# Kernel optimization log

Measured on AMD Instinct MI355X. Metric: run time of the kernel, lower is better.

## Reference

```python
import jax, jax.numpy as jnp
import numpy as np

# graph sizes
G, P, EP = 128, 256, 1024          # graphs, nodes/graph, edges/graph
N, E = G * P, G * EP
C, KENS, S = 4, 2, 1               # centroids, ensembles, samples
R = S * KENS                       # repeats
F, DE, D, OUT = 64, 16, 128, 10


def setup_inputs() -> dict:
    key = jax.random.key(0)
    ks = jax.random.split(key, 24)
    off = (jnp.arange(G, dtype=jnp.int32) * P)[:, None]
    src = (jax.random.randint(ks[0], (G, EP), 0, P, dtype=jnp.int32) + off).reshape(-1)
    dst = (jax.random.randint(ks[1], (G, EP), 0, P, dtype=jnp.int32) + off).reshape(-1)
    edge_index = jnp.stack([src, dst])            # [2, E], edges stay within graphs
    batch = jnp.repeat(jnp.arange(G, dtype=jnp.int32), P)  # [N]
    rn = lambda k, shp, s: jax.random.normal(k, shp, jnp.float32) * s
    return {
        "x_feat": rn(ks[2], (N, F), 1.0),
        "edge_attr": rn(ks[3], (E, DE), 1.0),
        "W_atom": rn(ks[4], (F, D), 0.1), "b_atom": jnp.zeros((D,), jnp.float32),
        "W_score": rn(ks[5], (D, C * KENS), 0.1),
        "W_edge": rn(ks[6], (DE, D), 0.1),
        "W_b2c": rn(ks[7], (D, D), 0.1),
        "W_bb": rn(ks[8], (D, D), 0.1), "W_bc": rn(ks[9], (D, D), 0.1),
        "W_cb": rn(ks[10], (D, D), 0.1), "W_cc": rn(ks[11], (D, D), 0.1),
        "W_sb": rn(ks[12], (D, D), 0.1), "W_sc": rn(ks[13], (D, D), 0.1),
        "W_inter": rn(ks[14], (D, D), 0.1), "b_inter": jnp.zeros((D,), jnp.float32),
        "W_out": rn(ks[15], (D, OUT), 0.1), "b_out": jnp.zeros((OUT,), jnp.float32),
        "edge_index": edge_index, "batch": batch,
    }


def reference(x_feat, edge_attr, W_atom, b_atom, W_score, W_edge, W_b2c,
              W_bb, W_bc, W_cb, W_cc, W_sb, W_sc, W_inter, b_inter,
              W_out, b_out, edge_index, batch):
    src, dst = edge_index[0], edge_index[1]
    # atom encoder + scorer + softmax sampler (marginals)
    x = x_feat @ W_atom + b_atom                                  # [N,D]
    scores = (x @ W_score).reshape(N, C, KENS)
    marg = jax.nn.softmax(scores, axis=1)                         # over centroids
    nm = jnp.broadcast_to(marg[None], (S, N, C, KENS))            # [S,N,C,KENS]
    nm = jnp.transpose(nm, (0, 3, 2, 1)).reshape(R, C, N)         # [R,C,N]
    em = nm[:, :, src] * nm[:, :, dst]                            # edge_mask [R,C,E]
    # base2centroid: masked MP on base graph + weighted segment-mean pooling
    edge_emb = edge_attr @ W_edge                                 # [E,D]
    h = jax.nn.relu(x @ W_b2c)                                    # [N,D]
    m = h[src] + edge_emb                                         # [E,D]
    agg = jnp.zeros((R, C, N, D), m.dtype).at[:, :, dst].add(em[..., None] * m)
    hm = h[None, None] + agg                                      # [R,C,N,D]
    denom = jnp.zeros((R, C, G), nm.dtype).at[:, :, batch].add(nm)
    num = jnp.zeros((R, C, G, D), hm.dtype).at[:, :, batch].add(nm[..., None] * hm)
    cent_x = jnp.transpose(num / (denom[..., None] + 1e-6), (0, 2, 1, 3))  # [R,G,C,D]
    # intra centroid-pair edge weights: triu pairs + diag, scatter over graphs
    iu, ju = np.triu_indices(C, 1)
    pi = np.concatenate([iu, np.arange(C)])
    pj = np.concatenate([ju, np.arange(C)])
    e2g = batch[src]
    w = jnp.zeros((R, pi.size, G), nm.dtype).at[:, :, e2g].add(
        nm[:, pi][:, :, src] * nm[:, pj][:, :, dst])              # [R,10,G]
    w = w.at[:, -C:, :].multiply(0.5)                             # halve diagonal counts
    wt = jnp.transpose(w, (0, 2, 1))                              # [R,G,10]
    Wcc = jnp.zeros((R, G, C, C), nm.dtype)
    Wcc = Wcc.at[:, :, pi, pj].add(wt).at[:, :, pj, pi].add(wt)   # to_undirected
    dg = jnp.arange(C)
    Wcc = Wcc.at[:, :, dg, dg].multiply(0.5)                      # self loops counted once
    Wcc = Wcc / (jax.lax.stop_gradient(jnp.max(Wcc)) + 1e-9)      # detached-max norm
    # hetero GNN layer: base->base, base->centroid, centroid->centroid, centroid->base
    agg_bb = jnp.zeros((N, D), x.dtype).at[dst].add(x[src] + edge_emb)           # [N,D]
    agg_bc = jnp.transpose(
        jnp.zeros((R, C, G, D), x.dtype).at[:, :, batch].add(nm[..., None] * x[None, None]),
        (0, 2, 1, 3))                                             # [R,G,C,D]
    agg_cc = jnp.einsum('rgij,rgjd->rgid', Wcc, cent_x)
    h_cent = jax.nn.relu(agg_bc @ W_bc + agg_cc @ W_cc + cent_x @ W_sc)          # [R,G,C,D]
    agg_cb = jnp.einsum('rcn,rncd->rnd', nm, h_cent[:, batch])                   # [R,N,D]
    h_base = jax.nn.relu(agg_bb[None] @ W_bb + agg_cb @ W_cb + x[None] @ W_sb)   # [R,N,D]
    # inter-ensemble mean pool, inter head, intra mean graph pool, intra head
    node_emb = jnp.mean(h_base, axis=0) @ W_inter + b_inter                      # [N,D]
    graph_emb = jnp.zeros((G, D), node_emb.dtype).at[batch].add(node_emb) / P    # [G,D]
    return graph_emb @ W_out + b_out                                             # [G,OUT]
```

## Files before the change

### kernel.cpp

```cpp
#include <hip/hip_runtime.h>
#include <hip/hip_bf16.h>

#define Nn 32768
#define Ee 131072
#define Gg 128
#define Dd 128

using bf16 = __hip_bfloat16;
typedef __attribute__((ext_vector_type(8))) short bf16x8;
typedef __attribute__((ext_vector_type(4))) float f32x4;

__device__ __forceinline__ float b2f(bf16 v){ return __bfloat162float(v); }
__device__ __forceinline__ bf16  f2b(float v){ return __float2bfloat16(v); }
__device__ __forceinline__ unsigned short bf16bits(float v){
  union { bf16 b; unsigned short u; } cv; cv.b = f2b(v); return cv.u;
}
__device__ __forceinline__ float bfu(unsigned short u){
  return __uint_as_float((unsigned int)u << 16);
}
__device__ __forceinline__ float upk_x(unsigned int v){ return __uint_as_float(v << 16); }
__device__ __forceinline__ float upk_h(unsigned int v){ return __uint_as_float(v & 0xffff0000u); }

__global__ __launch_bounds__(128)
void k_wrep(const float* __restrict__ Wbb, const float* __restrict__ Wsb,
            const float* __restrict__ Wcb, const float* __restrict__ Wa,
            const float* __restrict__ Wb2c,
            unsigned short* __restrict__ Wbbp, unsigned short* __restrict__ Wsbp,
            unsigned short* __restrict__ Wcbp, unsigned short* __restrict__ Wap,
            unsigned short* __restrict__ Wb2cp) {
  int mat = blockIdx.x >> 7, n = blockIdx.x & 127, k = threadIdx.x;
  if      (mat == 0) Wbbp [n*128 + k] = bf16bits(Wbb [k*128 + n]);
  else if (mat == 1) Wsbp [n*128 + k] = bf16bits(Wsb [k*128 + n]);
  else if (mat == 2) Wcbp [n*128 + k] = bf16bits(Wcb [k*128 + n]);
  else if (mat == 3) { if (k < 64) Wap[n*64 + k] = bf16bits(Wa[k*128 + n]); }
  else               Wb2cp[n*128 + k] = bf16bits(Wb2c[k*128 + n]);
}

__global__ __launch_bounds__(256)
void k_atom(const float* __restrict__ xf, const unsigned short* __restrict__ Wap,
            const float* __restrict__ ba, const float* __restrict__ Wsc,
            const unsigned short* __restrict__ Wb2cp,
            unsigned int* __restrict__ xh, float* __restrict__ nmt) {
  __shared__ unsigned short sxf[64*72];
  __shared__ unsigned short sxb[64*136];
  __shared__ float ss[64*8];
  __shared__ float sWsc[1024];
  int tid = threadIdx.x, n0 = blockIdx.x*64;
  int lane = tid & 63, wv = tid >> 6;
  int m = lane & 15, quad = lane >> 4;
  int rbase = wv*16;
  #pragma unroll
  for (int k = 0; k < 4; ++k) {
    int pos = (tid + k*256)*4;
    int node = pos >> 6, f = pos & 63;
    float4 v = *reinterpret_cast<const float4*>(xf + (size_t)n0*64 + pos);
    ushort4 o;
    o.x = bf16bits(v.x); o.y = bf16bits(v.y); o.z = bf16bits(v.z); o.w = bf16bits(v.w);
    *reinterpret_cast<ushort4*>(&sxf[node*72 + f]) = o;
  }
  for (int j = tid; j < 1024; j += 256) sWsc[j] = Wsc[j];
  __syncthreads();
  f32x4 cx[8];
  #pragma unroll
  for (int nt = 0; nt < 8; ++nt) {
    float bv = ba[nt*16 + m];
    cx[nt] = (f32x4){bv, bv, bv, bv};
  }
  const unsigned short* a1 = &sxf[(rbase + m)*72];
  #pragma unroll
  for (int nt = 0; nt < 8; ++nt) {
    #pragma unroll
    for (int kk = 0; kk < 2; ++kk) {
      int ko = kk*32 + quad*8;
      bf16x8 av = *reinterpret_cast<const bf16x8*>((const short*)a1 + ko);
      bf16x8 bv8 = *reinterpret_cast<const bf16x8*>((const short*)Wap + (nt*16 + m)*64 + ko);
      cx[nt] = __builtin_amdgcn_mfma_f32_16x16x32_bf16(av, bv8, cx[nt], 0, 0, 0);
    }
  }
  #pragma unroll
  for (int nt = 0; nt < 8; ++nt)
    #pragma unroll
    for (int i = 0; i < 4; ++i)
      sxb[(rbase + quad*4 + i)*136 + nt*16 + m] = bf16bits(cx[nt][i]);
  __syncthreads();
  for (int p = tid; p < 512; p += 256) {
    int node = p >> 3, col = p & 7;
    float s = 0.f;
    for (int dd = 0; dd < 128; ++dd)
      s += bfu(sxb[node*136 + dd]) * sWsc[dd*8 + col];
    ss[node*8 + col] = s;
  }
  __syncthreads();
  if (tid < 128) {
    int node = tid >> 1, k = tid & 1;
    float v0 = ss[node*8 + 0 + k], v1 = ss[node*8 + 2 + k];
    float v2 = ss[node*8 + 4 + k], v3 = ss[node*8 + 6 + k];
    float mx = fmaxf(fmaxf(v0, v1), fmaxf(v2, v3));
    float e0 = expf(v0-mx), e1 = expf(v1-mx), e2 = expf(v2-mx), e3 = expf(v3-mx);
    float inv = 1.f / (e0+e1+e2+e3);
    *reinterpret_cast<float4*>(nmt + (size_t)(n0 + node)*8 + k*4) =
        make_float4(e0*inv, e1*inv, e2*inv, e3*inv);
  }
  f32x4 chf[8];
  #pragma unroll
  for (int nt = 0; nt < 8; ++nt) chf[nt] = (f32x4){0.f,0.f,0.f,0.f};
  const unsigned short* a2 = &sxb[(rbase + m)*136];
  #pragma unroll
  for (int nt = 0; nt < 8; ++nt) {
    #pragma unroll
    for (int kk = 0; kk < 4; ++kk) {
      int ko = kk*32 + quad*8;
      bf16x8 av = *reinterpret_cast<const bf16x8*>((const short*)a2 + ko);
      bf16x8 bv8 = *reinterpret_cast<const bf16x8*>((const short*)Wb2cp + (nt*16 + m)*128 + ko);
      chf[nt] = __builtin_amdgcn_mfma_f32_16x16x32_bf16(av, bv8, chf[nt], 0, 0, 0);
    }
  }
  #pragma unroll
  for (int nt = 0; nt < 8; ++nt) {
    #pragma unroll
    for (int i = 0; i < 4; ++i) {
      int row = rbase + quad*4 + i, col = nt*16 + m;
      float hv = fmaxf(chf[nt][i], 0.f);
      unsigned short xb = sxb[row*136 + col];
      xh[(size_t)(n0 + row)*128 + col] =
          ((unsigned int)bf16bits(hv) << 16) | (unsigned int)xb;
    }
  }
}

__global__ __launch_bounds__(256)
void k_graph(const int* __restrict__ ei, const float* __restrict__ nmt,
             const float* __restrict__ ea,
             int* __restrict__ osrc, int* __restrict__ rowstart,
             float* __restrict__ sea, float* __restrict__ den,
             float* __restrict__ wcc, unsigned int* __restrict__ maxbits,
             float* __restrict__ bnm, float* __restrict__ gea) {
  __shared__ int sdl[1024], ssl[1024];
  __shared__ int cnt[256], off[256];
  __shared__ float eabuf[256*16];
  __shared__ float salpha[8*258];
  __shared__ float sbeta[8*256];
  __shared__ float seaacc[256*17];
  __shared__ float red[20];
  __shared__ float sga[256];
  __shared__ float den8[8];
  int t = threadIdx.x, g = blockIdx.x;
  cnt[t] = 0;
  for (int j = t; j < 2048; j += 256) sbeta[j] = 0.f;
  for (int j = t; j < 4352; j += 256) seaacc[j] = 0.f;
  if (t < 20) red[t] = 0.f;
  if (t < 8) den8[t] = 0.f;
  __syncthreads();
  #pragma unroll
  for (int j = 0; j < 4; ++j) {
    int e = t + j*256;
    int sl = ei[g*1024 + e] - g*256;
    int dl = ei[Ee + g*1024 + e] - g*256;
    ssl[e] = sl; sdl[e] = dl;
    atomicAdd(&cnt[dl], 1);
  }
  {
    const float4* p = reinterpret_cast<const float4*>(nmt + (size_t)(g*256 + t)*8);
    float4 a = p[0], b = p[1];
    float v[8] = {a.x,a.y,a.z,a.w,b.x,b.y,b.z,b.w};
    #pragma unroll
    for (int i = 0; i < 8; ++i) {
      float s = v[i];
      for (int o = 32; o > 0; o >>= 1) s += __shfl_xor(s, o);
      if ((t & 63) == 0) atomicAdd(&den8[i], s);
    }
  }
  __syncthreads();
  off[t] = cnt[t];
  __syncthreads();
  for (int s = 1; s < 256; s <<= 1) {
    int v = (t >= s) ? off[t - s] : 0;
    __syncthreads();
    off[t] += v;
    __syncthreads();
  }
  int startv = off[t] - cnt[t];
  rowstart[g*256 + t] = startv;
  off[t] = startv;
  __syncthreads();
  #pragma unroll
  for (int j = 0; j < 4; ++j) {
    int e = t + j*256;
    int pos = atomicAdd(&off[sdl[e]], 1);
    osrc[g*1024 + pos] = g*256 + ssl[e];
  }
  float w20[20];
  #pragma unroll
  for (int i = 0; i < 20; ++i) w20[i] = 0.f;
  float greg = 0.f;
  int grc = t >> 5, gj = (t >> 1) & 15, ghf = t & 1;
  for (int ch = 0; ch < 4; ++ch) {
    __syncthreads();
    for (int j = t; j < 1024; j += 256)
      reinterpret_cast<float4*>(eabuf)[j] =
        reinterpret_cast<const float4*>(ea + (size_t)(g*1024 + ch*256)*16)[j];
    {
      int e = ch*256 + t;
      int sl = ssl[e], dl = sdl[e];
      const float4* ps4 = reinterpret_cast<const float4*>(nmt + (size_t)(g*256 + sl)*8);
      const float4* pt4 = reinterpret_cast<const float4*>(nmt + (size_t)(g*256 + dl)*8);
      float4 sv0 = ps4[0], sv1 = ps4[1], tv0 = pt4[0], tv1 = pt4[1];
      float ps[8] = {sv0.x,sv0.y,sv0.z,sv0.w,sv1.x,sv1.y,sv1.z,sv1.w};
      float pt[8] = {tv0.x,tv0.y,tv0.z,tv0.w,tv1.x,tv1.y,tv1.z,tv1.w};
      #pragma unroll
      for (int r = 0; r < 2; ++r) {
        int b = r*4;
        w20[r*10+0] += ps[b+0]*pt[b+1]; w20[r*10+1] += ps[b+0]*pt[b+2];
        w20[r*10+2] += ps[b+0]*pt[b+3]; w20[r*10+3] += ps[b+1]*pt[b+2];
        w20[r*10+4] += ps[b+1]*pt[b+3]; w20[r*10+5] += ps[b+2]*pt[b+3];
        w20[r*10+6] += ps[b+0]*pt[b+0]; w20[r*10+7] += ps[b+1]*pt[b+1];
        w20[r*10+8] += ps[b+2]*pt[b+2]; w20[r*10+9] += ps[b+3]*pt[b+3];
      }
      #pragma unroll
      for (int rc = 0; rc < 8; ++rc) {
        float al = ps[rc]*pt[rc]*pt[rc];
        salpha[rc*258 + t] = al;
        atomicAdd(&sbeta[rc*256 + sl], al);
      }
    }
    __syncthreads();
    {
      int e = ch*256 + t;
      int dl = sdl[e];
      #pragma unroll
      for (int j2 = 0; j2 < 16; ++j2)
        atomicAdd(&seaacc[dl*17 + j2], eabuf[t*16 + j2]);
    }
    {
      float a = 0.f;
      int eb = ghf*128;
      for (int ee = eb; ee < eb + 128; ++ee)
        a += salpha[grc*258 + ee] * eabuf[ee*16 + gj];
      greg += a;
    }
  }
  #pragma unroll
  for (int i = 0; i < 20; ++i) {
    for (int o = 32; o > 0; o >>= 1) w20[i] += __shfl_down(w20[i], o);
  }
  if ((t & 63) == 0) {
    #pragma unroll
    for (int i = 0; i < 20; ++i) atomicAdd(&red[i], w20[i]);
  }
  sga[t] = greg;
  __syncthreads();
  if (t < 32) {
    int r = t >> 4, ij = t & 15, i = ij >> 2, j = ij & 3;
    float v;
    if (i == j) v = 0.5f * red[r*10 + 6 + i];
    else { int a = i < j ? i : j, b = i < j ? j : i;
           int p = (a == 0) ? (b - 1) : (a == 1) ? (b + 1) : 5;
           v = red[r*10 + p]; }
    wcc[(r*Gg + g)*16 + ij] = v;
    atomicMax(maxbits, __float_as_uint(v));
  }
  if ((t & 1) == 0) {
    float s = sga[t] + sga[t+1];
    gea[((size_t)grc*Gg + g)*16 + gj] = s;
  }
  {
    float4* bo = reinterpret_cast<float4*>(bnm + (size_t)(g*256 + t)*8);
    bo[0] = make_float4(sbeta[0*256+t], sbeta[1*256+t], sbeta[2*256+t], sbeta[3*256+t]);
    bo[1] = make_float4(sbeta[4*256+t], sbeta[5*256+t], sbeta[6*256+t], sbeta[7*256+t]);
  }
  {
    float4* so = reinterpret_cast<float4*>(sea + (size_t)(g*256 + t)*16);
    so[0] = make_float4(seaacc[t*17+0],  seaacc[t*17+1],  seaacc[t*17+2],  seaacc[t*17+3]);
    so[1] = make_float4(seaacc[t*17+4],  seaacc[t*17+5],  seaacc[t*17+6],  seaacc[t*17+7]);
    so[2] = make_float4(seaacc[t*17+8],  seaacc[t*17+9],  seaacc[t*17+10], seaacc[t*17+11]);
    so[3] = make_float4(seaacc[t*17+12], seaacc[t*17+13], seaacc[t*17+14], seaacc[t*17+15]);
  }
  if (t < 8) den[t*Gg + g] = den8[t];
}

__global__ __launch_bounds__(256)
void k_pool(const unsigned int* __restrict__ xh, const float* __restrict__ nmt,
            const float* __restrict__ bnm, float* __restrict__ pnum,
            float* __restrict__ pabc) {
  __shared__ float combN[8*128], combA[8*128];
  int t = threadIdx.x, d = t & 127, q = t >> 7;
  int g = blockIdx.x >> 4, e16 = blockIdx.x & 15;
  int nbase = g*256 + e16*16;
  float aH[8] = {0,0,0,0,0,0,0,0};
  float aX[8] = {0,0,0,0,0,0,0,0};
  for (int nn = q; nn < 16; nn += 2) {
    int n = nbase + nn;
    unsigned int vn = xh[(size_t)n*128 + d];
    float xn = upk_x(vn), hn = upk_h(vn);
    const float4* pp = reinterpret_cast<const float4*>(nmt + (size_t)n*8);
    float4 p0 = pp[0], p1 = pp[1];
    float pc[8] = {p0.x,p0.y,p0.z,p0.w,p1.x,p1.y,p1.z,p1.w};
    const float4* bp = reinterpret_cast<const float4*>(bnm + (size_t)n*8);
    float4 b0 = bp[0], b1 = bp[1];
    float bt[8] = {b0.x,b0.y,b0.z,b0.w,b1.x,b1.y,b1.z,b1.w};
    #pragma unroll
    for (int rc = 0; rc < 8; ++rc) {
      aH[rc] += (pc[rc] + bt[rc])*hn;
      aX[rc] += pc[rc]*xn;
    }
  }
  if (q == 1) {
    #pragma unroll
    for (int rc = 0; rc < 8; ++rc) { combN[rc*128+d] = aH[rc]; combA[rc*128+d] = aX[rc]; }
  }
  __syncthreads();
  if (q == 0) {
    #pragma unroll
    for (int rc = 0; rc < 8; ++rc) {
      pnum[(((size_t)rc*Gg + g)*16 + e16)*128 + d] = aH[rc] + combN[rc*128+d];
      pabc[(((size_t)rc*Gg + g)*16 + e16)*128 + d] = aX[rc] + combA[rc*128+d];
    }
  }
}

__global__ __launch_bounds__(256)
void k_aggx(const unsigned int* __restrict__ xh, const float* __restrict__ sea,
            const float* __restrict__ We, const int* __restrict__ osrc,
            const int* __restrict__ rowstart, unsigned short* __restrict__ aggbb16) {
  int t = threadIdx.x, d = t & 127, q = t >> 7;
  int g = blockIdx.x >> 5, e32 = blockIdx.x & 31;
  int nbase = g*256 + e32*8;
  float w[16];
  #pragma unroll
  for (int j = 0; j < 16; ++j) w[j] = We[j*128 + d];
  for (int nn = q; nn < 8; nn += 2) {
    int n = nbase + nn;
    const float4* sp = reinterpret_cast<const float4*>(sea + (size_t)n*16);
    float4 s0 = sp[0], s1 = sp[1], s2 = sp[2], s3 = sp[3];
    float agg = s0.x*w[0] + s0.y*w[1] + s0.z*w[2] + s0.w*w[3]
              + s1.x*w[4] + s1.y*w[5] + s1.z*w[6] + s1.w*w[7]
              + s2.x*w[8] + s2.y*w[9] + s2.z*w[10]+ s2.w*w[11]
              + s3.x*w[12]+ s3.y*w[13]+ s3.z*w[14]+ s3.w*w[15];
    int ln = n & 255;
    int start = rowstart[n];
    int end = (ln == 255) ? 1024 : rowstart[n+1];
    for (int jj = start; jj < end; ++jj) {
      int sg = osrc[g*1024 + jj];
      agg += upk_x(xh[(size_t)sg*128 + d]);
    }
    aggbb16[(size_t)n*128 + d] = bf16bits(agg);
  }
}

__global__ __launch_bounds__(128)
void k_hcent(const float* __restrict__ pnum, const float* __restrict__ den,
             const float* __restrict__ pabc, const float* __restrict__ gea,
             const float* __restrict__ We, const float* __restrict__ wcc,
             const unsigned int* __restrict__ maxbits,
             const float* __restrict__ Wbc, const float* __restrict__ Wcc_,
             const float* __restrict__ Wsc2, float* __restrict__ hcent) {
  __shared__ float scent[512], sbc[512], sccs[512], swcc[16];
  int tid = threadIdx.x, r = blockIdx.x >> 7, g = blockIdx.x & 127;
  float inv = 1.f / (__uint_as_float(*maxbits) + 1e-9f);
  if (tid < 16) swcc[tid] = wcc[(r*Gg + g)*16 + tid] * inv;
  for (int c = 0; c < 4; ++c) {
    int rc = r*4 + c;
    float nv = 0.f, av = 0.f;
    #pragma unroll
    for (int s = 0; s < 16; ++s) {
      nv += pnum[(((size_t)rc*Gg + g)*16 + s)*128 + tid];
      av += pabc[(((size_t)rc*Gg + g)*16 + s)*128 + tid];
    }
    const float* geag = gea + ((size_t)rc*Gg + g)*16;
    #pragma unroll
    for (int j = 0; j < 16; ++j) nv += geag[j] * We[j*128 + tid];
    float dn = den[rc*Gg + g] + 1e-6f;
    scent[c*128 + tid] = nv / dn;
    sbc[c*128 + tid]   = av;
  }
  __syncthreads();
  for (int i = 0; i < 4; ++i) {
    sccs[i*128 + tid] = swcc[i*4+0]*scent[tid]       + swcc[i*4+1]*scent[128 + tid]
                      + swcc[i*4+2]*scent[256 + tid] + swcc[i*4+3]*scent[384 + tid];
  }
  __syncthreads();
  float acc[4] = {0.f, 0.f, 0.f, 0.f};
  for (int k = 0; k < 128; ++k) {
    float wb = Wbc[k*128 + tid], wc = Wcc_[k*128 + tid], ws2 = Wsc2[k*128 + tid];
    #pragma unroll
    for (int c = 0; c < 4; ++c)
      acc[c] += sbc[c*128 + k]*wb + sccs[c*128 + k]*wc + scent[c*128 + k]*ws2;
  }
  #pragma unroll
  for (int c = 0; c < 4; ++c)
    hcent[((r*Gg + g)*4 + c)*128 + tid] = fmaxf(acc[c], 0.f);
}

__global__ __launch_bounds__(256)
void k_hbase(const unsigned short* __restrict__ aggbb16,
             const unsigned int* __restrict__ xh,
             const float* __restrict__ nmt, const float* __restrict__ hcent,
             const unsigned short* __restrict__ Wbbp,
             const unsigned short* __restrict__ Wsbp,
             const unsigned short* __restrict__ Wcbp,
             float* __restrict__ gsum) {
  __shared__ unsigned short A1[64*136];
  __shared__ unsigned short A2[64*136];
  __shared__ float shc[512];
  __shared__ float snm[256];
  __shared__ float pred[128];
  int tid = threadIdx.x, n0 = blockIdx.x*64, g = n0 >> 8;
  int lane = tid & 63, wv = tid >> 6;
  int m = lane & 15, quad = lane >> 4;
  int rbase = wv*16;
  for (int j = tid; j < 1024; j += 256) {
    int row = j >> 4, col = (j & 15) * 8;
    uint4 v = *reinterpret_cast<const uint4*>(aggbb16 + (size_t)(n0+row)*128 + col);
    *reinterpret_cast<uint4*>(&A1[row*136 + col]) = v;
  }
  for (int j = tid; j < 2048; j += 256) {
    int row = j >> 5, col = (j & 31) * 4;
    uint4 v = *reinterpret_cast<const uint4*>(xh + (size_t)(n0+row)*128 + col);
    uint2 o;
    o.x = (v.x & 0xffffu) | (v.y << 16);
    o.y = (v.z & 0xffffu) | (v.w << 16);
    *reinterpret_cast<uint2*>(&A2[row*136 + col]) = o;
  }
  __syncthreads();
  f32x4 bb[8];
  #pragma unroll
  for (int nt = 0; nt < 8; ++nt) bb[nt] = (f32x4){0.f,0.f,0.f,0.f};
  const short* a1r = (const short*)&A1[(rbase + m)*136];
  const short* a2r = (const short*)&A2[(rbase + m)*136];
  #pragma unroll
  for (int nt = 0; nt < 8; ++nt) {
    #pragma unroll
    for (int kk = 0; kk < 4; ++kk) {
      int ko = kk*32 + quad*8;
      bf16x8 av1 = *reinterpret_cast<const bf16x8*>(a1r + ko);
      bf16x8 wv1 = *reinterpret_cast<const bf16x8*>((const short*)Wbbp + (nt*16 + m)*128 + ko);
      bb[nt] = __builtin_amdgcn_mfma_f32_16x16x32_bf16(av1, wv1, bb[nt], 0, 0, 0);
      bf16x8 av2 = *reinterpret_cast<const bf16x8*>(a2r + ko);
      bf16x8 wv2 = *reinterpret_cast<const bf16x8*>((const short*)Wsbp + (nt*16 + m)*128 + ko);
      bb[nt] = __builtin_amdgcn_mfma_f32_16x16x32_bf16(av2, wv2, bb[nt], 0, 0, 0);
    }
  }
  __syncthreads();
  unsigned short* SB = A2;
  f32x4 msum[8];
  #pragma unroll
  for (int nt = 0; nt < 8; ++nt) msum[nt] = (f32x4){0.f,0.f,0.f,0.f};
  for (int r = 0; r < 2; ++r) {
    for (int j = tid; j < 512; j += 256) shc[j] = hcent[((size_t)(r*Gg + g)*4)*128 + j];
    if (tid < 256) snm[tid] = nmt[(size_t)(n0 + (tid >> 2))*8 + r*4 + (tid & 3)];
    __syncthreads();
    for (int j = tid; j < 8192; j += 256) {
      int node = j >> 7, k = j & 127;
      float v = snm[node*4+0]*shc[k]       + snm[node*4+1]*shc[128 + k]
              + snm[node*4+2]*shc[256 + k] + snm[node*4+3]*shc[384 + k];
      SB[node*136 + k] = bf16bits(v);
    }
    __syncthreads();
    f32x4 aw[8];
    #pragma unroll
    for (int nt = 0; nt < 8; ++nt) aw[nt] = (f32x4){0.f,0.f,0.f,0.f};
    const short* sbr = (const short*)&SB[(rbase + m)*136];
    #pragma unroll
    for (int nt = 0; nt < 8; ++nt) {
      #pragma unroll
      for (int kk = 0; kk < 4; ++kk) {
        int ko = kk*32 + quad*8;
        bf16x8 av = *reinterpret_cast<const bf16x8*>(sbr + ko);
        bf16x8 wvv = *reinterpret_cast<const bf16x8*>((const short*)Wcbp + (nt*16 + m)*128 + ko);
        aw[nt] = __builtin_amdgcn_mfma_f32_16x16x32_bf16(av, wvv, aw[nt], 0, 0, 0);
      }
    }
    #pragma unroll
    for (int nt = 0; nt < 8; ++nt) {
      #pragma unroll
      for (int i = 0; i < 4; ++i)
        msum[nt][i] += 0.5f * fmaxf(bb[nt][i] + aw[nt][i], 0.f);
    }
    __syncthreads();
  }
  if (tid < 128) pred[tid] = 0.f;
  __syncthreads();
  #pragma unroll
  for (int nt = 0; nt < 8; ++nt) {
    float s = msum[nt][0] + msum[nt][1] + msum[nt][2] + msum[nt][3];
    atomicAdd(&pred[nt*16 + m], s);
  }
  __syncthreads();
  if (tid < 128) atomicAdd(&gsum[g*128 + tid], pred[tid]);
}

__global__ __launch_bounds__(128)
void k_out(const float* __restrict__ gsum, const float* __restrict__ Wint,
           const float* __restrict__ bint, const float* __restrict__ Wout,
           const float* __restrict__ bout, float* __restrict__ out) {
  __shared__ float ss[128], sge[128];
  int tid = threadIdx.x, g = blockIdx.x;
  ss[tid] = gsum[g*128 + tid] * (1.f/256.f);
  __syncthreads();
  float ge = bint[tid];
  for (int k = 0; k < 128; ++k) ge += ss[k] * Wint[k*128 + tid];
  sge[tid] = ge;
  __syncthreads();
  if (tid < 10) {
    float o = bout[tid];
    for (int d = 0; d < 128; ++d) o += sge[d] * Wout[d*10 + tid];
    out[g*10 + tid] = o;
  }
}

extern "C" void kernel_launch(void* const* d_in, const int* in_sizes, int n_in,
                              void* d_out, int out_size, void* d_ws, size_t ws_size,
                              hipStream_t stream) {
  const float* xf   = (const float*)d_in[0];
  const float* ea   = (const float*)d_in[1];
  const float* Wa   = (const float*)d_in[2];
  const float* ba   = (const float*)d_in[3];
  const float* Wsc  = (const float*)d_in[4];
  const float* We   = (const float*)d_in[5];
  const float* Wb2c = (const float*)d_in[6];
  const float* Wbb  = (const float*)d_in[7];
  const float* Wbc  = (const float*)d_in[8];
  const float* Wcb  = (const float*)d_in[9];
  const float* WccW = (const float*)d_in[10];
  const float* Wsb  = (const float*)d_in[11];
  const float* Wsc2 = (const float*)d_in[12];
  const float* Wint = (const float*)d_in[13];
  const float* bint = (const float*)d_in[14];
  const float* Wout = (const float*)d_in[15];
  const float* bout = (const float*)d_in[16];
  const int*   ei   = (const int*)d_in[17];

  float* ws    = (float*)d_ws;
  unsigned int* xh = (unsigned int*)ws;
  float* nmt   = ws + 4194304;
  float* hcent = ws + 4456448;
  float* wcc   = ws + 4587520;
  unsigned short* aggbb16 = (unsigned short*)(ws + 4591616);
  int*   osrc  = (int*)(ws + 6688768);
  int*   rowst = (int*)(ws + 6819840);
  float* sea   = ws + 6852608;
  float* bnm   = ws + 7376896;
  float* gea   = ws + 7639040;
  float* pnum  = ws + 7655424;
  float* pabc  = ws + 9752576;
  float* den   = ws + 11849728;
  float* gsum  = ws + 11850752;
  unsigned int* maxbits = (unsigned int*)(ws + 11867136);
  unsigned short* Wbbp  = (unsigned short*)(ws + 11867200);
  unsigned short* Wsbp  = (unsigned short*)(ws + 11875392);
  unsigned short* Wcbp  = (unsigned short*)(ws + 11883584);
  unsigned short* Wap   = (unsigned short*)(ws + 11891776);
  unsigned short* Wb2cp = (unsigned short*)(ws + 11895872);

  hipMemsetAsync(gsum, 0, (16384 + 64) * sizeof(float), stream);

  k_wrep <<<5*128, 128, 0, stream>>>(Wbb, Wsb, Wcb, Wa, Wb2c,
                                     Wbbp, Wsbp, Wcbp, Wap, Wb2cp);
  k_atom <<<Nn/64, 256, 0, stream>>>(xf, Wap, ba, Wsc, Wb2cp, xh, nmt);
  k_graph<<<Gg,    256, 0, stream>>>(ei, nmt, ea, osrc, rowst, sea, den,
                                     wcc, maxbits, bnm, gea);
  k_pool <<<Gg*16, 256, 0, stream>>>(xh, nmt, bnm, pnum, pabc);
  k_aggx <<<Gg*32, 256, 0, stream>>>(xh, sea, We, osrc, rowst, aggbb16);
  k_hcent<<<2*Gg,  128, 0, stream>>>(pnum, den, pabc, gea, We, wcc, maxbits,
                                     Wbc, WccW, Wsc2, hcent);
  k_hbase<<<Nn/64, 256, 0, stream>>>(aggbb16, xh, nmt, hcent, Wbbp, Wsbp, Wcbp, gsum);
  k_out  <<<Gg,    128, 0, stream>>>(gsum, Wint, bint, Wout, bout, (float*)d_out);
}
```

Baseline: 294.6 us.

## Split per-graph edge kernel into CSR, edge-partial, gather and finalize kernels

The monolithic per-graph k_graph kernel, which ran only 128 blocks, is split into four kernels. k_csr builds the CSR with edge ids. k_edge runs 4 blocks per graph and writes partial beta, gea and Wcc sums. k_sea replaces shared-memory atomics with a CSR gather of edge attributes, and k_wfin computes the Wcc normalisation max deterministically. Consumers now sum the 4 partials, and per-block graph sums replace the global atomics and memset. This raises parallelism and removes atomic contention, at the cost of extra launches and partial-buffer traffic.

```diff
diff --git a/kernel.cpp b/kernel.cpp
--- a/kernel.cpp
+++ b/kernel.cpp
@@ -129,26 +129,13 @@
 }
 
 __global__ __launch_bounds__(256)
-void k_graph(const int* __restrict__ ei, const float* __restrict__ nmt,
-             const float* __restrict__ ea,
-             int* __restrict__ osrc, int* __restrict__ rowstart,
-             float* __restrict__ sea, float* __restrict__ den,
-             float* __restrict__ wcc, unsigned int* __restrict__ maxbits,
-             float* __restrict__ bnm, float* __restrict__ gea) {
-  __shared__ int sdl[1024], ssl[1024];
-  __shared__ int cnt[256], off[256];
-  __shared__ float eabuf[256*16];
-  __shared__ float salpha[8*258];
-  __shared__ float sbeta[8*256];
-  __shared__ float seaacc[256*17];
-  __shared__ float red[20];
-  __shared__ float sga[256];
+void k_csr(const int* __restrict__ ei, const float* __restrict__ nmt,
+           int* __restrict__ osrc, int* __restrict__ oeid,
+           int* __restrict__ rowstart, float* __restrict__ den) {
+  __shared__ int cnt[256], off[256], sdl[1024], ssl[1024];
   __shared__ float den8[8];
   int t = threadIdx.x, g = blockIdx.x;
   cnt[t] = 0;
-  for (int j = t; j < 2048; j += 256) sbeta[j] = 0.f;
-  for (int j = t; j < 4352; j += 256) seaacc[j] = 0.f;
-  if (t < 20) red[t] = 0.f;
   if (t < 8) den8[t] = 0.f;
   __syncthreads();
   #pragma unroll
@@ -188,55 +175,58 @@
     int e = t + j*256;
     int pos = atomicAdd(&off[sdl[e]], 1);
     osrc[g*1024 + pos] = g*256 + ssl[e];
-  }
+    oeid[g*1024 + pos] = e;
+  }
+  if (t < 8) den[t*Gg + g] = den8[t];
+}
+
+__global__ __launch_bounds__(256)
+void k_edge(const int* __restrict__ ei, const float* __restrict__ nmt,
+            const float* __restrict__ ea, float* __restrict__ bnmp,
+            float* __restrict__ geap, float* __restrict__ wsump) {
+  __shared__ float eaT[16*260];
+  __shared__ float salT[8*260];
+  __shared__ float sbeta[8*260];
+  __shared__ float red[20];
+  __shared__ float sga[256];
+  int t = threadIdx.x, bq = blockIdx.x;
+  int g = bq >> 2;
+  int ebase = g*1024 + (bq & 3)*256;
+  for (int j = t; j < 2080; j += 256) sbeta[j] = 0.f;
+  if (t < 20) red[t] = 0.f;
+  __syncthreads();
+  int sl = ei[ebase + t] - g*256;
+  int dl = ei[Ee + ebase + t] - g*256;
+  const float4* ps4 = reinterpret_cast<const float4*>(nmt + (size_t)(g*256 + sl)*8);
+  const float4* pt4 = reinterpret_cast<const float4*>(nmt + (size_t)(g*256 + dl)*8);
+  float4 sv0 = ps4[0], sv1 = ps4[1], tv0 = pt4[0], tv1 = pt4[1];
+  float ps[8] = {sv0.x,sv0.y,sv0.z,sv0.w,sv1.x,sv1.y,sv1.z,sv1.w};
+  float pt[8] = {tv0.x,tv0.y,tv0.z,tv0.w,tv1.x,tv1.y,tv1.z,tv1.w};
   float w20[20];
   #pragma unroll
-  for (int i = 0; i < 20; ++i) w20[i] = 0.f;
-  float greg = 0.f;
-  int grc = t >> 5, gj = (t >> 1) & 15, ghf = t & 1;
-  for (int ch = 0; ch < 4; ++ch) {
-    __syncthreads();
-    for (int j = t; j < 1024; j += 256)
-      reinterpret_cast<float4*>(eabuf)[j] =
-        reinterpret_cast<const float4*>(ea + (size_t)(g*1024 + ch*256)*16)[j];
-    {
-      int e = ch*256 + t;
-      int sl = ssl[e], dl = sdl[e];
-      const float4* ps4 = reinterpret_cast<const float4*>(nmt + (size_t)(g*256 + sl)*8);
-      const float4* pt4 = reinterpret_cast<const float4*>(nmt + (size_t)(g*256 + dl)*8);
-      float4 sv0 = ps4[0], sv1 = ps4[1], tv0 = pt4[0], tv1 = pt4[1];
-      float ps[8] = {sv0.x,sv0.y,sv0.z,sv0.w,sv1.x,sv1.y,sv1.z,sv1.w};
-      float pt[8] = {tv0.x,tv0.y,tv0.z,tv0.w,tv1.x,tv1.y,tv1.z,tv1.w};
-      #pragma unroll
-      for (int r = 0; r < 2; ++r) {
-        int b = r*4;
-        w20[r*10+0] += ps[b+0]*pt[b+1]; w20[r*10+1] += ps[b+0]*pt[b+2];
-        w20[r*10+2] += ps[b+0]*pt[b+3]; w20[r*10+3] += ps[b+1]*pt[b+2];
-        w20[r*10+4] += ps[b+1]*pt[b+3]; w20[r*10+5] += ps[b+2]*pt[b+3];
-        w20[r*10+6] += ps[b+0]*pt[b+0]; w20[r*10+7] += ps[b+1]*pt[b+1];
-        w20[r*10+8] += ps[b+2]*pt[b+2]; w20[r*10+9] += ps[b+3]*pt[b+3];
-      }
-      #pragma unroll
-      for (int rc = 0; rc < 8; ++rc) {
-        float al = ps[rc]*pt[rc]*pt[rc];
-        salpha[rc*258 + t] = al;
-        atomicAdd(&sbeta[rc*256 + sl], al);
-      }
-    }
-    __syncthreads();
-    {
-      int e = ch*256 + t;
-      int dl = sdl[e];
-      #pragma unroll
-      for (int j2 = 0; j2 < 16; ++j2)
-        atomicAdd(&seaacc[dl*17 + j2], eabuf[t*16 + j2]);
-    }
-    {
-      float a = 0.f;
-      int eb = ghf*128;
-      for (int ee = eb; ee < eb + 128; ++ee)
-        a += salpha[grc*258 + ee] * eabuf[ee*16 + gj];
-      greg += a;
+  for (int r = 0; r < 2; ++r) {
+    int b = r*4;
+    w20[r*10+0] = ps[b+0]*pt[b+1]; w20[r*10+1] = ps[b+0]*pt[b+2];
+    w20[r*10+2] = ps[b+0]*pt[b+3]; w20[r*10+3] = ps[b+1]*pt[b+2];
+    w20[r*10+4] = ps[b+1]*pt[b+3]; w20[r*10+5] = ps[b+2]*pt[b+3];
+    w20[r*10+6] = ps[b+0]*pt[b+0]; w20[r*10+7] = ps[b+1]*pt[b+1];
+    w20[r*10+8] = ps[b+2]*pt[b+2]; w20[r*10+9] = ps[b+3]*pt[b+3];
+  }
+  #pragma unroll
+  for (int rc = 0; rc < 8; ++rc) {
+    float al = ps[rc]*pt[rc]*pt[rc];
+    salT[rc*260 + t] = al;
+    atomicAdd(&sbeta[rc*260 + sl], al);
+  }
+  {
+    const float4* ea4 = reinterpret_cast<const float4*>(ea + (size_t)ebase*16);
+    #pragma unroll
+    for (int k = 0; k < 4; ++k) {
+      float4 v = ea4[t*4 + k];
+      eaT[(k*4+0)*260 + t] = v.x;
+      eaT[(k*4+1)*260 + t] = v.y;
+      eaT[(k*4+2)*260 + t] = v.z;
+      eaT[(k*4+3)*260 + t] = v.w;
     }
   }
   #pragma unroll
@@ -247,40 +237,82 @@
     #pragma unroll
     for (int i = 0; i < 20; ++i) atomicAdd(&red[i], w20[i]);
   }
-  sga[t] = greg;
-  __syncthreads();
-  if (t < 32) {
-    int r = t >> 4, ij = t & 15, i = ij >> 2, j = ij & 3;
-    float v;
-    if (i == j) v = 0.5f * red[r*10 + 6 + i];
-    else { int a = i < j ? i : j, b = i < j ? j : i;
-           int p = (a == 0) ? (b - 1) : (a == 1) ? (b + 1) : 5;
-           v = red[r*10 + p]; }
-    wcc[(r*Gg + g)*16 + ij] = v;
-    atomicMax(maxbits, __float_as_uint(v));
-  }
+  __syncthreads();
+  {
+    int rc = t >> 5, j = (t >> 1) & 15, hf = t & 1;
+    float a = 0.f;
+    int eb = hf*128;
+    for (int ee = eb; ee < eb + 128; ++ee)
+      a += salT[rc*260 + ee] * eaT[j*260 + ee];
+    sga[t] = a;
+  }
+  __syncthreads();
   if ((t & 1) == 0) {
-    float s = sga[t] + sga[t+1];
-    gea[((size_t)grc*Gg + g)*16 + gj] = s;
-  }
+    int rc = t >> 5, j = (t >> 1) & 15;
+    geap[(size_t)bq*128 + rc*16 + j] = sga[t] + sga[t+1];
+  }
+  if (t < 20) wsump[bq*20 + t] = red[t];
   {
-    float4* bo = reinterpret_cast<float4*>(bnm + (size_t)(g*256 + t)*8);
-    bo[0] = make_float4(sbeta[0*256+t], sbeta[1*256+t], sbeta[2*256+t], sbeta[3*256+t]);
-    bo[1] = make_float4(sbeta[4*256+t], sbeta[5*256+t], sbeta[6*256+t], sbeta[7*256+t]);
-  }
-  {
-    float4* so = reinterpret_cast<float4*>(sea + (size_t)(g*256 + t)*16);
-    so[0] = make_float4(seaacc[t*17+0],  seaacc[t*17+1],  seaacc[t*17+2],  seaacc[t*17+3]);
-    so[1] = make_float4(seaacc[t*17+4],  seaacc[t*17+5],  seaacc[t*17+6],  seaacc[t*17+7]);
-    so[2] = make_float4(seaacc[t*17+8],  seaacc[t*17+9],  seaacc[t*17+10], seaacc[t*17+11]);
-    so[3] = make_float4(seaacc[t*17+12], seaacc[t*17+13], seaacc[t*17+14], seaacc[t*17+15]);
-  }
-  if (t < 8) den[t*Gg + g] = den8[t];
+    float4* bo = reinterpret_cast<float4*>(bnmp + (size_t)bq*2048 + t*8);
+    bo[0] = make_float4(sbeta[0*260+t], sbeta[1*260+t], sbeta[2*260+t], sbeta[3*260+t]);
+    bo[1] = make_float4(sbeta[4*260+t], sbeta[5*260+t], sbeta[6*260+t], sbeta[7*260+t]);
+  }
+}
+
+__global__ __launch_bounds__(256)
+void k_sea(const float* __restrict__ ea, const int* __restrict__ oeid,
+           const int* __restrict__ rowstart, float* __restrict__ sea) {
+  int t = threadIdx.x;
+  int n = blockIdx.x*16 + (t >> 4);
+  int j = t & 15;
+  int g = n >> 8;
+  int start = rowstart[n];
+  int end = ((n & 255) == 255) ? 1024 : rowstart[n+1];
+  float s = 0.f;
+  for (int jj = start; jj < end; ++jj) {
+    int e = oeid[g*1024 + jj];
+    s += ea[((size_t)g*1024 + e)*16 + j];
+  }
+  sea[(size_t)n*16 + j] = s;
+}
+
+__global__ __launch_bounds__(128)
+void k_wfin(const float* __restrict__ wsump, float* __restrict__ wcc,
+            float* __restrict__ maxv) {
+  __shared__ float smax[128];
+  int t = threadIdx.x;
+  float w[20];
+  #pragma unroll
+  for (int i = 0; i < 20; ++i)
+    w[i] = wsump[(t*4+0)*20 + i] + wsump[(t*4+1)*20 + i]
+         + wsump[(t*4+2)*20 + i] + wsump[(t*4+3)*20 + i];
+  float mx = 0.f;
+  #pragma unroll
+  for (int r = 0; r < 2; ++r) {
+    #pragma unroll
+    for (int ij = 0; ij < 16; ++ij) {
+      int i = ij >> 2, j = ij & 3;
+      float v;
+      if (i == j) v = 0.5f * w[r*10 + 6 + i];
+      else { int a = i < j ? i : j, b = i < j ? j : i;
+             int p = (a == 0) ? (b - 1) : (a == 1) ? (b + 1) : 5;
+             v = w[r*10 + p]; }
+      wcc[(r*Gg + t)*16 + ij] = v;
+      mx = fmaxf(mx, v);
+    }
+  }
+  smax[t] = mx;
+  __syncthreads();
+  for (int s = 64; s > 0; s >>= 1) {
+    if (t < s) smax[t] = fmaxf(smax[t], smax[t + s]);
+    __syncthreads();
+  }
+  if (t == 0) maxv[0] = smax[0];
 }
 
 __global__ __launch_bounds__(256)
 void k_pool(const unsigned int* __restrict__ xh, const float* __restrict__ nmt,
-            const float* __restrict__ bnm, float* __restrict__ pnum,
+            const float* __restrict__ bnmp, float* __restrict__ pnum,
             float* __restrict__ pabc) {
   __shared__ float combN[8*128], combA[8*128];
   int t = threadIdx.x, d = t & 127, q = t >> 7;
@@ -290,14 +322,20 @@
   float aX[8] = {0,0,0,0,0,0,0,0};
   for (int nn = q; nn < 16; nn += 2) {
     int n = nbase + nn;
+    int ln = n & 255;
     unsigned int vn = xh[(size_t)n*128 + d];
     float xn = upk_x(vn), hn = upk_h(vn);
     const float4* pp = reinterpret_cast<const float4*>(nmt + (size_t)n*8);
     float4 p0 = pp[0], p1 = pp[1];
     float pc[8] = {p0.x,p0.y,p0.z,p0.w,p1.x,p1.y,p1.z,p1.w};
-    const float4* bp = reinterpret_cast<const float4*>(bnm + (size_t)n*8);
-    float4 b0 = bp[0], b1 = bp[1];
-    float bt[8] = {b0.x,b0.y,b0.z,b0.w,b1.x,b1.y,b1.z,b1.w};
+    float bt[8] = {0,0,0,0,0,0,0,0};
+    #pragma unroll
+    for (int qq = 0; qq < 4; ++qq) {
+      const float4* bp = reinterpret_cast<const float4*>(bnmp + (size_t)(g*4+qq)*2048 + ln*8);
+      float4 b0 = bp[0], b1 = bp[1];
+      bt[0]+=b0.x; bt[1]+=b0.y; bt[2]+=b0.z; bt[3]+=b0.w;
+      bt[4]+=b1.x; bt[5]+=b1.y; bt[6]+=b1.z; bt[7]+=b1.w;
+    }
     #pragma unroll
     for (int rc = 0; rc < 8; ++rc) {
       aH[rc] += (pc[rc] + bt[rc])*hn;
@@ -349,15 +387,22 @@
 
 __global__ __launch_bounds__(128)
 void k_hcent(const float* __restrict__ pnum, const float* __restrict__ den,
-             const float* __restrict__ pabc, const float* __restrict__ gea,
+             const float* __restrict__ pabc, const float* __restrict__ geap,
              const float* __restrict__ We, const float* __restrict__ wcc,
-             const unsigned int* __restrict__ maxbits,
+             const float* __restrict__ maxv,
              const float* __restrict__ Wbc, const float* __restrict__ Wcc_,
              const float* __restrict__ Wsc2, float* __restrict__ hcent) {
-  __shared__ float scent[512], sbc[512], sccs[512], swcc[16];
+  __shared__ float scent[512], sbc[512], sccs[512], swcc[16], sgea[64];
   int tid = threadIdx.x, r = blockIdx.x >> 7, g = blockIdx.x & 127;
-  float inv = 1.f / (__uint_as_float(*maxbits) + 1e-9f);
+  float inv = 1.f / (maxv[0] + 1e-9f);
   if (tid < 16) swcc[tid] = wcc[(r*Gg + g)*16 + tid] * inv;
+  if (tid < 64) {
+    int c = tid >> 4, j = tid & 15;
+    int idx = (r*4 + c)*16 + j;
+    sgea[tid] = geap[(size_t)(g*4+0)*128 + idx] + geap[(size_t)(g*4+1)*128 + idx]
+              + geap[(size_t)(g*4+2)*128 + idx] + geap[(size_t)(g*4+3)*128 + idx];
+  }
+  __syncthreads();
   for (int c = 0; c < 4; ++c) {
     int rc = r*4 + c;
     float nv = 0.f, av = 0.f;
@@ -366,9 +411,8 @@
       nv += pnum[(((size_t)rc*Gg + g)*16 + s)*128 + tid];
       av += pabc[(((size_t)rc*Gg + g)*16 + s)*128 + tid];
     }
-    const float* geag = gea + ((size_t)rc*Gg + g)*16;
-    #pragma unroll
-    for (int j = 0; j < 16; ++j) nv += geag[j] * We[j*128 + tid];
+    #pragma unroll
+    for (int j = 0; j < 16; ++j) nv += sgea[c*16 + j] * We[j*128 + tid];
     float dn = den[rc*Gg + g] + 1e-6f;
     scent[c*128 + tid] = nv / dn;
     sbc[c*128 + tid]   = av;
@@ -398,7 +442,7 @@
              const unsigned short* __restrict__ Wbbp,
              const unsigned short* __restrict__ Wsbp,
              const unsigned short* __restrict__ Wcbp,
-             float* __restrict__ gsum) {
+             float* __restrict__ pgsum) {
   __shared__ unsigned short A1[64*136];
   __shared__ unsigned short A2[64*136];
   __shared__ float shc[512];
@@ -486,16 +530,18 @@
     atomicAdd(&pred[nt*16 + m], s);
   }
   __syncthreads();
-  if (tid < 128) atomicAdd(&gsum[g*128 + tid], pred[tid]);
+  if (tid < 128) pgsum[(size_t)blockIdx.x*128 + tid] = pred[tid];
 }
 
 __global__ __launch_bounds__(128)
-void k_out(const float* __restrict__ gsum, const float* __restrict__ Wint,
+void k_out(const float* __restrict__ pgsum, const float* __restrict__ Wint,
            const float* __restrict__ bint, const float* __restrict__ Wout,
            const float* __restrict__ bout, float* __restrict__ out) {
   __shared__ float ss[128], sge[128];
   int tid = threadIdx.x, g = blockIdx.x;
-  ss[tid] = gsum[g*128 + tid] * (1.f/256.f);
+  float s = pgsum[(size_t)(g*4+0)*128 + tid] + pgsum[(size_t)(g*4+1)*128 + tid]
+          + pgsum[(size_t)(g*4+2)*128 + tid] + pgsum[(size_t)(g*4+3)*128 + tid];
+  ss[tid] = s * (1.f/256.f);
   __syncthreads();
   float ge = bint[tid];
   for (int k = 0; k < 128; ++k) ge += ss[k] * Wint[k*128 + tid];
@@ -537,32 +583,34 @@
   float* wcc   = ws + 4587520;
   unsigned short* aggbb16 = (unsigned short*)(ws + 4591616);
   int*   osrc  = (int*)(ws + 6688768);
-  int*   rowst = (int*)(ws + 6819840);
-  float* sea   = ws + 6852608;
-  float* bnm   = ws + 7376896;
-  float* gea   = ws + 7639040;
-  float* pnum  = ws + 7655424;
-  float* pabc  = ws + 9752576;
-  float* den   = ws + 11849728;
-  float* gsum  = ws + 11850752;
-  unsigned int* maxbits = (unsigned int*)(ws + 11867136);
-  unsigned short* Wbbp  = (unsigned short*)(ws + 11867200);
-  unsigned short* Wsbp  = (unsigned short*)(ws + 11875392);
-  unsigned short* Wcbp  = (unsigned short*)(ws + 11883584);
-  unsigned short* Wap   = (unsigned short*)(ws + 11891776);
-  unsigned short* Wb2cp = (unsigned short*)(ws + 11895872);
-
-  hipMemsetAsync(gsum, 0, (16384 + 64) * sizeof(float), stream);
+  int*   oeid  = (int*)(ws + 6819840);
+  int*   rowst = (int*)(ws + 6950912);
+  float* sea   = ws + 6983680;
+  float* bnmp  = ws + 7507968;
+  float* geap  = ws + 8556544;
+  float* wsump = ws + 8622080;
+  float* pnum  = ws + 8632320;
+  float* pabc  = ws + 10729472;
+  float* den   = ws + 12826624;
+  float* pgsum = ws + 12827648;
+  float* maxv  = ws + 12893184;
+  unsigned short* Wbbp  = (unsigned short*)(ws + 12893248);
+  unsigned short* Wsbp  = (unsigned short*)(ws + 12901440);
+  unsigned short* Wcbp  = (unsigned short*)(ws + 12909632);
+  unsigned short* Wap   = (unsigned short*)(ws + 12917824);
+  unsigned short* Wb2cp = (unsigned short*)(ws + 12921920);
 
   k_wrep <<<5*128, 128, 0, stream>>>(Wbb, Wsb, Wcb, Wa, Wb2c,
                                      Wbbp, Wsbp, Wcbp, Wap, Wb2cp);
   k_atom <<<Nn/64, 256, 0, stream>>>(xf, Wap, ba, Wsc, Wb2cp, xh, nmt);
-  k_graph<<<Gg,    256, 0, stream>>>(ei, nmt, ea, osrc, rowst, sea, den,
-                                     wcc, maxbits, bnm, gea);
-  k_pool <<<Gg*16, 256, 0, stream>>>(xh, nmt, bnm, pnum, pabc);
+  k_csr  <<<Gg,    256, 0, stream>>>(ei, nmt, osrc, oeid, rowst, den);
+  k_edge <<<Gg*4,  256, 0, stream>>>(ei, nmt, ea, bnmp, geap, wsump);
+  k_sea  <<<Nn/16, 256, 0, stream>>>(ea, oeid, rowst, sea);
+  k_wfin <<<1,     128, 0, stream>>>(wsump, wcc, maxv);
+  k_pool <<<Gg*16, 256, 0, stream>>>(xh, nmt, bnmp, pnum, pabc);
   k_aggx <<<Gg*32, 256, 0, stream>>>(xh, sea, We, osrc, rowst, aggbb16);
-  k_hcent<<<2*Gg,  128, 0, stream>>>(pnum, den, pabc, gea, We, wcc, maxbits,
+  k_hcent<<<2*Gg,  128, 0, stream>>>(pnum, den, pabc, geap, We, wcc, maxv,
                                      Wbc, WccW, Wsc2, hcent);
-  k_hbase<<<Nn/64, 256, 0, stream>>>(aggbb16, xh, nmt, hcent, Wbbp, Wsbp, Wcbp, gsum);
-  k_out  <<<Gg,    128, 0, stream>>>(gsum, Wint, bint, Wout, bout, (float*)d_out);
-}
+  k_hbase<<<Nn/64, 256, 0, stream>>>(aggbb16, xh, nmt, hcent, Wbbp, Wsbp, Wcbp, pgsum);
+  k_out  <<<Gg,    128, 0, stream>>>(pgsum, Wint, bint, Wout, bout, (float*)d_out);
+}
```

Result: faster. 281.2 us (-4.6%).
